# Optimization experiments

Measured on AMD Instinct MI355X. Metric: run time of the kernel, lower is better.

The kernel has to match this reference:

```python
import jax, jax.numpy as jnp
import numpy as np

DIM, DEPTH, DH, H, NLAT, MAXT, MAXF, FFM = 1024, 6, 64, 8, 64, 8, 16, 4
INNER = DH * H

def _ln(x, w, b, eps=1e-5):
    m = jnp.mean(x, axis=-1, keepdims=True)
    v = jnp.mean(jnp.square(x - m), axis=-1, keepdims=True)
    return (x - m) * jax.lax.rsqrt(v + eps) * w + b

def setup_inputs() -> dict:
    key = jax.random.key(0)
    ks = iter(jax.random.split(key, 32))
    s = 0.02
    d = {
        'x': jax.random.normal(next(ks), (2, 8, 16, 256, DIM), jnp.float32),
        'latents': jax.random.normal(next(ks), (NLAT, DIM), jnp.float32),
        'frame_emb': jax.random.normal(next(ks), (MAXF, DIM), jnp.float32),
        'media_emb': jax.random.normal(next(ks), (MAXT, 1, DIM), jnp.float32),
        'lnm_w': jnp.ones((DEPTH, DIM)), 'lnm_b': jnp.zeros((DEPTH, DIM)),
        'lnl_w': jnp.ones((DEPTH, DIM)), 'lnl_b': jnp.zeros((DEPTH, DIM)),
        'Wq': jax.random.normal(next(ks), (DEPTH, DIM, INNER), jnp.float32) * s,
        'Wkv': jax.random.normal(next(ks), (DEPTH, DIM, 2 * INNER), jnp.float32) * s,
        'Wo': jax.random.normal(next(ks), (DEPTH, INNER, DIM), jnp.float32) * s,
        'ffln_w': jnp.ones((DEPTH, DIM)), 'ffln_b': jnp.zeros((DEPTH, DIM)),
        'W1': jax.random.normal(next(ks), (DEPTH, DIM, FFM * DIM), jnp.float32) * s,
        'b1': jnp.zeros((DEPTH, FFM * DIM)),
        'W2': jax.random.normal(next(ks), (DEPTH, FFM * DIM, DIM), jnp.float32) * s,
        'b2': jnp.zeros((DEPTH, DIM)),
        'fln_w': jnp.ones((DIM,)), 'fln_b': jnp.zeros((DIM,)),
    }
    return d

def _split_heads(t):  # b T n (h d) -> b h T n d
    b, T, n, _ = t.shape
    return t.reshape(b, T, n, H, DH).transpose(0, 3, 1, 2, 4)

def _forward(x, latents, frame_emb, media_emb, lnm_w, lnm_b, lnl_w, lnl_b,
             Wq, Wkv, Wo, ffln_w, ffln_b, W1, b1, W2, b2, fln_w, fln_b):
    b, T, F, v, d = x.shape
    x = x + frame_emb[:F][None, None, :, None, :]      # b T F v d
    x = x.reshape(b, T, F * v, d)
    x = x + media_emb[:T]                              # [T,1,d] broadcasts
    lat = jnp.broadcast_to(latents, (b, T, NLAT, d))
    scale = DH ** -0.5
    for i in range(DEPTH):
        xn = _ln(x, lnm_w[i], lnm_b[i])
        ln_lat = _ln(lat, lnl_w[i], lnl_b[i])
        q = _split_heads(ln_lat @ Wq[i]) * scale       # b h T n2 dh
        kv = jnp.concatenate([xn, ln_lat], axis=2) @ Wkv[i]
        k, vv = jnp.split(kv, 2, axis=-1)
        k, vv = _split_heads(k), _split_heads(vv)      # b h T (n1+n2) dh
        sim = jnp.einsum('bhtid,bhtjd->bhtij', q, k)
        sim = sim - jax.lax.stop_gradient(jnp.max(sim, axis=-1, keepdims=True))
        attn = jax.nn.softmax(sim, axis=-1)
        o = jnp.einsum('bhtij,bhtjd->bhtid', attn, vv)
        o = o.transpose(0, 2, 3, 1, 4).reshape(b, T, NLAT, INNER)
        lat = (o @ Wo[i]) + lat
        h = _ln(lat, ffln_w[i], ffln_b[i])
        h = jax.nn.gelu(h @ W1[i] + b1[i], approximate=False) @ W2[i] + b2[i]
        lat = h + lat
    return _ln(lat, fln_w, fln_b)

def reference(x, latents, frame_emb, media_emb, lnm_w, lnm_b, lnl_w, lnl_b,
              Wq, Wkv, Wo, ffln_w, ffln_b, W1, b1, W2, b2, fln_w, fln_b):
    return _forward(x, latents, frame_emb, media_emb, lnm_w, lnm_b, lnl_w, lnl_b,
                    Wq, Wkv, Wo, ffln_w, ffln_b, W1, b1, W2, b2, fln_w, fln_b)
```

## Files before the change

kernel.cpp:

```cpp
#include <hip/hip_runtime.h>
#include <math.h>


#define DIM   1024
#define DEPTH 6
#define HEADS 8
#define NLAT  64
#define INNER 512
#define FFD   4096
#define XROWS 65536
#define LROWS 1024
#define NBT   16
#define QKVN  1536

typedef __attribute__((ext_vector_type(8))) short bf16x8;
typedef __attribute__((ext_vector_type(4))) float f32x4;

#define WAITV(n) asm volatile("s_waitcnt vmcnt(" #n ")" ::: "memory")

__device__ __forceinline__ short f2bf(float f) {
  union { float f; unsigned u; } v; v.f = f;
  unsigned r = v.u + 0x7fffu + ((v.u >> 16) & 1u);
  return (short)(r >> 16);
}

__device__ __forceinline__ void gload16(const void* g, void* l) {
  __builtin_amdgcn_global_load_lds(
      (const __attribute__((address_space(1))) unsigned int*)g,
      (__attribute__((address_space(3))) unsigned int*)l, 16, 0, 0);
}

__device__ __forceinline__ f32x4 zero_f4() { f32x4 z; z[0]=0.f; z[1]=0.f; z[2]=0.f; z[3]=0.f; return z; }
__device__ __forceinline__ bf16x8 zero_b8() { bf16x8 z;
#pragma unroll
  for (int e=0;e<8;e++) z[e]=0; return z; }

__global__ __launch_bounds__(256)
void prep_kernel(const float* __restrict__ x, const float* __restrict__ fe,
                 const float* __restrict__ me, short* __restrict__ xhat)
{
  int lane = threadIdx.x & 63;
  int r = blockIdx.x*4 + (threadIdx.x >> 6);
  int f = (r >> 8) & 15, tt = (r >> 12) & 7;
  const float4* xp = (const float4*)(x + (size_t)r*DIM);
  const float4* fp = (const float4*)(fe + (size_t)f*DIM);
  const float4* mp = (const float4*)(me + (size_t)tt*DIM);
  float y[16];
  float s = 0.f, sq = 0.f;
#pragma unroll
  for (int k = 0; k < 4; k++) {
    float4 xv = xp[k*64 + lane], fv = fp[k*64 + lane], mv = mp[k*64 + lane];
    float a0 = xv.x+fv.x+mv.x, a1 = xv.y+fv.y+mv.y, a2 = xv.z+fv.z+mv.z, a3 = xv.w+fv.w+mv.w;
    y[k*4+0]=a0; y[k*4+1]=a1; y[k*4+2]=a2; y[k*4+3]=a3;
    s += a0+a1+a2+a3; sq += a0*a0+a1*a1+a2*a2+a3*a3;
  }
#pragma unroll
  for (int off = 32; off >= 1; off >>= 1) {
    s  += __shfl_xor(s,  off, 64);
    sq += __shfl_xor(sq, off, 64);
  }
  float mean = s * (1.0f/DIM);
  float var  = sq * (1.0f/DIM) - mean*mean;
  float rs = rsqrtf(var + 1e-5f);
  short4* op = (short4*)(xhat + (size_t)r*DIM);
#pragma unroll
  for (int k = 0; k < 4; k++) {
    short4 o;
    o.x = f2bf((y[k*4+0]-mean)*rs); o.y = f2bf((y[k*4+1]-mean)*rs);
    o.z = f2bf((y[k*4+2]-mean)*rs); o.w = f2bf((y[k*4+3]-mean)*rs);
    op[k*64 + lane] = o;
  }
}

__device__ __forceinline__ void reduce2(float& s, float& sq, float* sh) {
#pragma unroll
  for (int off = 32; off >= 1; off >>= 1) {
    s  += __shfl_xor(s,  off, 64);
    sq += __shfl_xor(sq, off, 64);
  }
  int t = threadIdx.x;
  if ((t & 63) == 0) { sh[(t >> 6)*2] = s; sh[(t >> 6)*2 + 1] = sq; }
  __syncthreads();
  s  = sh[0] + sh[2] + sh[4] + sh[6];
  sq = sh[1] + sh[3] + sh[5] + sh[7];
}

template<bool OBF>
__global__ __launch_bounds__(256)
void ln_kernel(const float* __restrict__ in, const float* __restrict__ w,
               const float* __restrict__ b, void* __restrict__ outp)
{
  __shared__ float sh[8];
  int r = blockIdx.x, t = threadIdx.x;
  float4 xv = ((const float4*)(in + (size_t)r*DIM))[t];
  float s = xv.x+xv.y+xv.z+xv.w;
  float sq = xv.x*xv.x+xv.y*xv.y+xv.z*xv.z+xv.w*xv.w;
  reduce2(s, sq, sh);
  float mean = s*(1.0f/DIM), var = sq*(1.0f/DIM) - mean*mean;
  float rs = rsqrtf(var + 1e-5f);
  float4 wv = ((const float4*)w)[t], bv = ((const float4*)b)[t];
  float o0 = (xv.x-mean)*rs*wv.x + bv.x;
  float o1 = (xv.y-mean)*rs*wv.y + bv.y;
  float o2 = (xv.z-mean)*rs*wv.z + bv.z;
  float o3 = (xv.w-mean)*rs*wv.w + bv.w;
  if (OBF) {
    short4 o; o.x=f2bf(o0); o.y=f2bf(o1); o.z=f2bf(o2); o.w=f2bf(o3);
    ((short4*)((short*)outp + (size_t)r*DIM))[t] = o;
  } else {
    float4 o; o.x=o0; o.y=o1; o.z=o2; o.w=o3;
    ((float4*)((float*)outp + (size_t)r*DIM))[t] = o;
  }
}

__global__ __launch_bounds__(256)
void latinit_kernel(const float* __restrict__ latents, float* __restrict__ lat)
{
  int idx = blockIdx.x * 256 + threadIdx.x;
  int e = idx << 2;
  int row = e >> 10;
  int i = row & 63;
  int col = e & 1023;
  *(float4*)(lat + e) = *(const float4*)(latents + (i << 10) + col);
}

__global__ __launch_bounds__(256)
void kvbp_kernel(const float* __restrict__ lnm_b, const float* __restrict__ Wkv,
                 float* __restrict__ kvb_part)
{
  int z = blockIdx.x, i = blockIdx.y, t = threadIdx.x;
  const float* W = Wkv + (size_t)i*DIM*DIM;
  const float* bv = lnm_b + (size_t)i*DIM;
  float acc0=0,acc1=0,acc2=0,acc3=0;
  for (int k = z*64; k < z*64+64; k++) {
    float b = bv[k];
    const float* Wr = W + (size_t)k*DIM;
    acc0 += b * Wr[t];       acc1 += b * Wr[t+256];
    acc2 += b * Wr[t+512];   acc3 += b * Wr[t+768];
  }
  float* o = kvb_part + (size_t)(i*16 + z)*DIM;
  o[t] = acc0; o[t+256] = acc1; o[t+512] = acc2; o[t+768] = acc3;
}

__global__ __launch_bounds__(256)
void kvbred_kernel(const float* __restrict__ kvb_part, float* __restrict__ kvb)
{
  int i = blockIdx.x, t = threadIdx.x;
#pragma unroll
  for (int j = 0; j < 4; j++) {
    int col = t + j*256;
    float s = 0.f;
#pragma unroll
    for (int z = 0; z < 16; z++) s += kvb_part[(size_t)(i*16 + z)*DIM + col];
    kvb[i*DIM + col] = s;
  }
}

__global__ __launch_bounds__(256)
void tcast_all_kernel(const float* __restrict__ Wkv, const float* __restrict__ Wq,
                      const float* __restrict__ Wo, const float* __restrict__ W1,
                      const float* __restrict__ W2, const float* __restrict__ lnmw,
                      short* __restrict__ Wkv_f, short* __restrict__ qkvW,
                      short* __restrict__ Wo_h, short* __restrict__ W1_h,
                      short* __restrict__ W2_h)
{
  int b = blockIdx.x;
  const float* src; short* dst; const float* fold = nullptr; float scale = 1.0f;
  int K, N, bx, ntx;
  if (b < 256)      { src=Wkv; dst=Wkv_f; fold=lnmw; K=1024; N=1024; bx=b;      ntx=16; }
  else if (b < 384) { src=Wq;  dst=qkvW;  scale=0.125f; K=1024; N=512; bx=b-256; ntx=8; }
  else if (b < 640) { src=Wkv; dst=qkvW+512*1024; K=1024; N=1024; bx=b-384; ntx=16; }
  else if (b < 768) { src=Wo;  dst=Wo_h;  K=512;  N=1024; bx=b-640; ntx=16; }
  else if (b < 1792){ src=W1;  dst=W1_h;  K=1024; N=4096; bx=b-768; ntx=64; }
  else              { src=W2;  dst=W2_h;  K=4096; N=1024; bx=b-1792; ntx=16; }
  int n0 = (bx % ntx)*64, k0 = (bx / ntx)*64;
  __shared__ float tile[64][65];
  int t = threadIdx.x;
#pragma unroll
  for (int i = 0; i < 16; i++) {
    int rr = (t >> 6) + i*4, cc = t & 63;
    float v = src[(size_t)(k0+rr)*N + n0 + cc] * scale;
    if (fold) v *= fold[k0 + rr];
    tile[rr][cc] = v;
  }
  __syncthreads();
#pragma unroll
  for (int i = 0; i < 16; i++) {
    int nn = (t >> 6) + i*4, kk = t & 63;
    dst[(size_t)(n0+nn)*K + k0 + kk] = f2bf(tile[kk][nn]);
  }
}

__global__ __launch_bounds__(512, 1)
void gemm256p_kernel(const short* __restrict__ A, const short* __restrict__ Bt,
                     short* __restrict__ C, const float* __restrict__ bias,
                     int M, int N, int K)
{
  __shared__ __align__(16) short lds[65536];
  char* ldsc = (char*)lds;
  const int t = threadIdx.x, lane = t & 63, wid = t >> 6;
  const int wm = wid >> 2, wn = wid & 3;

  const int nwg = gridDim.x * gridDim.y;
  const int id = blockIdx.y * gridDim.x + blockIdx.x;
  const int work = (id & 7) * (nwg >> 3) + (id >> 3);
  const int bn = work % gridDim.x, bm = work / gridDim.x;
  const int m0 = bm * 256, n0 = bn * 256;

  f32x4 acc[8][4];
#pragma unroll
  for (int m=0;m<8;m++)
#pragma unroll
    for (int n=0;n<4;n++) acc[m][n] = zero_f4();

  auto stage = [&](int tile, int mat, int half) {
    const short* src = mat ? Bt : A;
    const int base0 = (mat ? n0 : m0) + half*128;
    char* dbase = ldsc + (mat*32768 + (tile & 1)*16384 + half*8192)*2;
#pragma unroll
    for (int i = 0; i < 2; i++) {
      int chunk = i*512 + t;
      int row_h = chunk >> 3, slot = chunk & 7;
      int ss = slot ^ (row_h & 7);
      gload16(src + (size_t)(base0 + row_h)*K + tile*64 + ss*8,
              dbase + (i*512 + (wid << 6))*16);
    }
  };
  auto LDA = [&](int buf, int mf, int ks) -> bf16x8 {
    int row = wm*128 + mf*16 + (lane & 15);
    int slot = (ks*4 + (lane >> 4)) ^ (row & 7);
    return *(const bf16x8*)(ldsc + (buf*16384 + row*64)*2 + slot*16);
  };
  auto LDB = [&](int buf, int nf, int ks) -> bf16x8 {
    int row = wn*64 + nf*16 + (lane & 15);
    int slot = (ks*4 + (lane >> 4)) ^ (row & 7);
    return *(const bf16x8*)(ldsc + (32768 + buf*16384 + row*64)*2 + slot*16);
  };

#define PHASE(BUF, Q, STAGE_STMT, GATE) do {                               \
    if ((Q) == 0) {                                                        \
      _Pragma("unroll") for (int n_=0;n_<4;n_++)                           \
        _Pragma("unroll") for (int k_=0;k_<2;k_++)                         \
          bfr[n_][k_] = LDB((BUF), n_, k_);                                \
    }                                                                      \
    _Pragma("unroll") for (int i_=0;i_<2;i_++)                             \
      _Pragma("unroll") for (int k_=0;k_<2;k_++)                           \
        afr[i_][k_] = LDA((BUF), 2*(Q)+i_, k_);                            \
    STAGE_STMT;                                                            \
    GATE;                                                                  \
    __builtin_amdgcn_sched_barrier(0);                                     \
    __builtin_amdgcn_s_barrier();                                          \
    asm volatile("s_waitcnt lgkmcnt(0)" ::: "memory");                     \
    __builtin_amdgcn_sched_barrier(0);                                     \
    __builtin_amdgcn_s_setprio(1);                                         \
    _Pragma("unroll") for (int k_=0;k_<2;k_++)                             \
      _Pragma("unroll") for (int i_=0;i_<2;i_++)                           \
        _Pragma("unroll") for (int n_=0;n_<4;n_++)                         \
          acc[2*(Q)+i_][n_] = __builtin_amdgcn_mfma_f32_16x16x32_bf16(     \
              afr[i_][k_], bfr[n_][k_], acc[2*(Q)+i_][n_], 0, 0, 0);       \
    __builtin_amdgcn_s_setprio(0);                                         \
    __builtin_amdgcn_sched_barrier(0);                                     \
    __builtin_amdgcn_s_barrier();                                          \
  } while (0)

  const int NU = K >> 7;
  stage(0, 0, 0); stage(0, 0, 1); stage(0, 1, 0); stage(0, 1, 1);
  stage(1, 1, 0); stage(1, 1, 1);
  WAITV(4);
  __builtin_amdgcn_sched_barrier(0);
  __builtin_amdgcn_s_barrier();

#pragma unroll 1
  for (int u = 0; u < NU; ++u) {
    const int t0 = 2*u, t1 = t0 + 1;
    const bool more = (u + 1 < NU);
    bf16x8 bfr[4][2], afr[2][2];
    PHASE(0, 0, stage(t1, 0, 0),               (void)0);
    PHASE(0, 1, stage(t1, 0, 1),               (void)0);
    PHASE(0, 2, if (more) stage(t0+2, 1, 0),   (void)0);
    PHASE(0, 3, if (more) stage(t0+2, 1, 1),   WAITV(4));
    PHASE(1, 0, if (more) stage(t0+2, 0, 0),   (void)0);
    PHASE(1, 1, if (more) stage(t0+2, 0, 1),   (void)0);
    PHASE(1, 2, if (more) stage(t1+2, 1, 0),   (void)0);
    PHASE(1, 3, if (more) stage(t1+2, 1, 1),   WAITV(4));
  }
#undef PHASE

  const int g = lane >> 4;
#pragma unroll
  for (int m=0;m<8;m++) {
#pragma unroll
    for (int n=0;n<4;n++) {
#pragma unroll
      for (int r=0;r<4;r++) {
        int mm = m0 + wm*128 + m*16 + g*4 + r;
        int nn = n0 + wn*64 + n*16 + (lane & 15);
        float v = acc[m][n][r] + bias[nn];
        C[(size_t)mm*N + nn] = f2bf(v);
      }
    }
  }
}

template<int EPI, bool HAS_BIAS>
__global__ __launch_bounds__(256, 2)
void gemm_kernel(const short* __restrict__ A, const short* __restrict__ Bt,
                 void* __restrict__ Cout, const float* __restrict__ bias,
                 int M, int N, int K, int ldk)
{
  __shared__ __align__(16) short As[128*64];
  __shared__ __align__(16) short Bs[128*64];
  const int t = threadIdx.x;
  const int lane = t & 63, w = t >> 6;
  const int m0 = blockIdx.x * 128, n0 = blockIdx.y * 128;
  const int wr = (w >> 1) * 64, wc = (w & 1) * 64;
  const short* Ap = A + (size_t)blockIdx.z * K;
  const short* Btp = Bt + (size_t)blockIdx.z * K;

  f32x4 acc[4][4];
#pragma unroll
  for (int i=0;i<4;i++)
#pragma unroll
    for (int j=0;j<4;j++) acc[i][j] = zero_f4();

  for (int kt = 0; kt < K; kt += 64) {
#pragma unroll
    for (int i = 0; i < 4; i++) {
      int chunk = i*256 + t;
      int row = chunk >> 3, slot = chunk & 7;
      int ss = slot ^ (row & 7);
      gload16(Ap + (size_t)(m0 + row)*ldk + kt + ss*8,
              (char*)As + (i*256 + (w<<6))*16);
    }
#pragma unroll
    for (int i = 0; i < 4; i++) {
      int chunk = i*256 + t;
      int row = chunk >> 3, slot = chunk & 7;
      int ss = slot ^ (row & 7);
      gload16(Btp + (size_t)(n0 + row)*ldk + kt + ss*8,
              (char*)Bs + (i*256 + (w<<6))*16);
    }
    __syncthreads();

#pragma unroll
    for (int ks = 0; ks < 2; ks++) {
      bf16x8 af[4], bfr[4];
#pragma unroll
      for (int i=0;i<4;i++) {
        int row = wr + i*16 + (lane & 15);
        int slot = (ks*4 + (lane >> 4)) ^ (row & 7);
        af[i] = *(const bf16x8*)((const char*)As + row*128 + slot*16);
        int nrow = wc + i*16 + (lane & 15);
        int nslot = (ks*4 + (lane >> 4)) ^ (nrow & 7);
        bfr[i] = *(const bf16x8*)((const char*)Bs + nrow*128 + nslot*16);
      }
#pragma unroll
      for (int i=0;i<4;i++)
#pragma unroll
        for (int j=0;j<4;j++)
          acc[i][j] = __builtin_amdgcn_mfma_f32_16x16x32_bf16(af[i], bfr[j], acc[i][j], 0, 0, 0);
    }
    __syncthreads();
  }

  const int g = lane >> 4;
#pragma unroll
  for (int i=0;i<4;i++) {
#pragma unroll
    for (int j=0;j<4;j++) {
#pragma unroll
      for (int r=0;r<4;r++) {
        int m = m0 + wr + i*16 + g*4 + r;
        int n = n0 + wc + j*16 + (lane & 15);
        float v = acc[i][j][r];
        if (EPI == 0) {
          if (HAS_BIAS) v += bias[n];
          ((short*)Cout)[(size_t)m*N + n] = f2bf(v);
        } else if (EPI == 1) {
          if (HAS_BIAS) v += bias[n];
          float gl = 0.5f * v * (1.0f + erff(v * 0.70710678f));
          ((short*)Cout)[(size_t)m*N + n] = f2bf(gl);
        } else if (EPI == 2) {
          if (HAS_BIAS) v += bias[n];
          float* o = (float*)Cout + (size_t)m*N + n;
          *o += v;
        } else {
          ((float*)Cout)[(size_t)blockIdx.z*M*N + (size_t)m*N + n] = v;
        }
      }
    }
  }
}

__global__ __launch_bounds__(256)
void w2red_kernel(const float* __restrict__ part, const float* __restrict__ b2,
                  float* __restrict__ lat)
{
  int idx = blockIdx.x * 256 + threadIdx.x;
  float4 a = ((float4*)lat)[idx];
  float4 bb = ((const float4*)b2)[idx & 255];
  a.x += bb.x; a.y += bb.y; a.z += bb.z; a.w += bb.w;
#pragma unroll
  for (int z = 0; z < 4; z++) {
    float4 p = ((const float4*)(part + (size_t)z*LROWS*DIM))[idx];
    a.x += p.x; a.y += p.y; a.z += p.z; a.w += p.w;
  }
  ((float4*)lat)[idx] = a;
}

__global__ __launch_bounds__(256, 2)
void attn_part_kernel(const short* __restrict__ qkvlat, const short* __restrict__ kvbuf,
                      float* __restrict__ part_O, float* __restrict__ part_m,
                      float* __restrict__ part_l)
{
  __shared__ __align__(16) short q_sh[64*64];
  __shared__ __align__(16) short K_sh[128*64];
  __shared__ __align__(16) short VT_sh[64*128];
  __shared__ __align__(16) short P_sh[64*132];

  const int t = threadIdx.x, lane = t & 63, w = t >> 6;
  const int bid = blockIdx.x;
  const int s = bid & 7, bh = bid >> 3;
  const int h = bh & 7, bt = bh >> 3;

  {
    const short* qsrc = qkvlat + (size_t)(bt*64)*QKVN + h*64;
#pragma unroll
    for (int i = 0; i < 2; i++) {
      int chunk = i*256 + t;
      int row = chunk >> 3, slot = chunk & 7;
      gload16(qsrc + (size_t)row*QKVN + ((slot ^ (row & 7))*8),
              (char*)q_sh + (i*256 + (w<<6))*16);
    }
  }

  float m_run[4], l_run[4];
#pragma unroll
  for (int r=0;r<4;r++){ m_run[r] = -1e30f; l_run[r] = 0.f; }
  f32x4 oacc[4];
#pragma unroll
  for (int j=0;j<4;j++) oacc[j] = zero_f4();

  const int nch = (s == 7) ? 5 : 4;
  for (int c5 = 0; c5 < nch; c5++) {
    __syncthreads();
    const bool isLat = (c5 == 4);
    const int jv = isLat ? 4 : 8;
    const short* kbase; int kstride, valid;
    if (!isLat) {
      kbase = kvbuf + ((size_t)bt*4096 + (s*4 + c5)*128)*DIM + h*64;
      kstride = DIM; valid = 128;
    } else {
      kbase = qkvlat + (size_t)(bt*64)*QKVN + 512 + h*64;
      kstride = QKVN; valid = 64;
    }
    const short* vbase = kbase + 512;

#pragma unroll
    for (int i = 0; i < 4; i++) {
      int chunk = i*256 + t;
      int row = chunk >> 3, slot = chunk & 7;
      gload16(kbase + (size_t)row*kstride + ((slot ^ (row & 7))*8),
              (char*)K_sh + (i*256 + (w<<6))*16);
    }
#pragma unroll
    for (int i = 0; i < 4; i++) {
      int c = i*256 + t;
      int row = c >> 3, slot = c & 7;
      bf16x8 v = (row < valid) ? *(const bf16x8*)(vbase + (size_t)row*kstride + slot*8) : zero_b8();
      int kslot = row >> 3;
#pragma unroll
      for (int e=0;e<8;e++) {
        int dh = slot*8 + e;
        VT_sh[dh*128 + ((kslot ^ (dh & 7))*8) + (row & 7)] = v[e];
      }
    }
    __syncthreads();

    f32x4 sacc[8];
#pragma unroll
    for (int j=0;j<8;j++) sacc[j] = zero_f4();
#pragma unroll
    for (int ks=0; ks<2; ks++) {
      int arow = w*16 + (lane & 15);
      int aslot = (ks*4 + (lane >> 4)) ^ (arow & 7);
      bf16x8 af = *(const bf16x8*)((const char*)q_sh + arow*128 + aslot*16);
#pragma unroll
      for (int j=0;j<8;j++) {
        int brow = j*16 + (lane & 15);
        int bslot = (ks*4 + (lane >> 4)) ^ (brow & 7);
        bf16x8 bv = *(const bf16x8*)((const char*)K_sh + brow*128 + bslot*16);
        sacc[j] = __builtin_amdgcn_mfma_f32_16x16x32_bf16(af, bv, sacc[j], 0, 0, 0);
      }
    }

    float mx[4];
#pragma unroll
    for (int r=0;r<4;r++) mx[r] = -1e30f;
#pragma unroll
    for (int j=0;j<8;j++) {
      if (j < jv) {
#pragma unroll
        for (int r=0;r<4;r++) mx[r] = fmaxf(mx[r], sacc[j][r]);
      }
    }
#pragma unroll
    for (int m2=1; m2<16; m2<<=1) {
#pragma unroll
      for (int r=0;r<4;r++) mx[r] = fmaxf(mx[r], __shfl_xor(mx[r], m2, 64));
    }
    float alpha[4], rowsum[4];
#pragma unroll
    for (int r=0;r<4;r++) {
      float nm = fmaxf(m_run[r], mx[r]);
      alpha[r] = __expf(m_run[r] - nm);
      m_run[r] = nm;
      rowsum[r] = 0.f;
    }
#pragma unroll
    for (int j=0;j<8;j++) {
#pragma unroll
      for (int r=0;r<4;r++) {
        float p = 0.f;
        if (j < jv) { p = __expf(sacc[j][r] - m_run[r]); rowsum[r] += p; }
        P_sh[(w*16 + (lane>>4)*4 + r)*132 + j*16 + (lane & 15)] = f2bf(p);
      }
    }
#pragma unroll
    for (int m2=1; m2<16; m2<<=1) {
#pragma unroll
      for (int r=0;r<4;r++) rowsum[r] += __shfl_xor(rowsum[r], m2, 64);
    }
#pragma unroll
    for (int r=0;r<4;r++) l_run[r] = l_run[r]*alpha[r] + rowsum[r];
#pragma unroll
    for (int j=0;j<4;j++) {
#pragma unroll
      for (int r=0;r<4;r++) oacc[j][r] *= alpha[r];
    }
    __syncthreads();

#pragma unroll
    for (int ks=0; ks<4; ks++) {
      int prow = w*16 + (lane & 15);
      bf16x8 af = *(const bf16x8*)((const char*)P_sh + prow*264 + ks*64 + (lane >> 4)*16);
#pragma unroll
      for (int j=0;j<4;j++) {
        int dh = j*16 + (lane & 15);
        int kslot = (ks*4 + (lane >> 4)) ^ (dh & 7);
        bf16x8 bv = *(const bf16x8*)((const char*)VT_sh + dh*256 + kslot*16);
        oacc[j] = __builtin_amdgcn_mfma_f32_16x16x32_bf16(af, bv, oacc[j], 0, 0, 0);
      }
    }
  }

  {
    float* Ob = part_O + (size_t)bid*4096;
    int rbase = w*16 + (lane>>4)*4;
#pragma unroll
    for (int j=0;j<4;j++) {
#pragma unroll
      for (int r=0;r<4;r++)
        Ob[(rbase + r)*64 + j*16 + (lane & 15)] = oacc[j][r];
    }
    if ((lane & 15) == 0) {
#pragma unroll
      for (int r=0;r<4;r++) {
        part_m[(size_t)bid*64 + rbase + r] = m_run[r];
        part_l[(size_t)bid*64 + rbase + r] = l_run[r];
      }
    }
  }
}

__global__ __launch_bounds__(256)
void attn_combine_kernel(const float* __restrict__ part_O, const float* __restrict__ part_m,
                         const float* __restrict__ part_l, short* __restrict__ obuf)
{
  int bh = blockIdx.x, t = threadIdx.x;
  int q = t >> 2, c0 = (t & 3) * 16;
  int bt = bh >> 3, h = bh & 7;
  float m8[8], w8[8];
  float mmax = -1e30f;
#pragma unroll
  for (int s=0;s<8;s++) { m8[s] = part_m[(size_t)(bh*8+s)*64 + q]; mmax = fmaxf(mmax, m8[s]); }
  float lt = 0.f;
#pragma unroll
  for (int s=0;s<8;s++) { w8[s] = __expf(m8[s] - mmax); lt += w8[s] * part_l[(size_t)(bh*8+s)*64 + q]; }
  float inv = 1.0f / lt;
  float4 acc[4];
#pragma unroll
  for (int u=0;u<4;u++) { acc[u].x=0.f; acc[u].y=0.f; acc[u].z=0.f; acc[u].w=0.f; }
#pragma unroll
  for (int s=0;s<8;s++) {
    const float4* Ob = (const float4*)(part_O + ((size_t)(bh*8+s)*64 + q)*64 + c0);
#pragma unroll
    for (int u=0;u<4;u++) {
      float4 v = Ob[u];
      acc[u].x += w8[s]*v.x; acc[u].y += w8[s]*v.y;
      acc[u].z += w8[s]*v.z; acc[u].w += w8[s]*v.w;
    }
  }
  short* ob = obuf + (size_t)(bt*64 + q)*INNER + h*64 + c0;
#pragma unroll
  for (int u=0;u<4;u++) {
    short4 o;
    o.x = f2bf(acc[u].x*inv); o.y = f2bf(acc[u].y*inv);
    o.z = f2bf(acc[u].z*inv); o.w = f2bf(acc[u].w*inv);
    ((short4*)ob)[u] = o;
  }
}

extern "C" void kernel_launch(void* const* d_in, const int* in_sizes, int n_in,
                              void* d_out, int out_size, void* d_ws, size_t ws_size,
                              hipStream_t stream)
{
  (void)in_sizes; (void)n_in; (void)out_size; (void)ws_size;
  const float* x        = (const float*)d_in[0];
  const float* latents  = (const float*)d_in[1];
  const float* frame_e  = (const float*)d_in[2];
  const float* media_e  = (const float*)d_in[3];
  const float* lnm_w    = (const float*)d_in[4];
  const float* lnm_b    = (const float*)d_in[5];
  const float* lnl_w    = (const float*)d_in[6];
  const float* lnl_b    = (const float*)d_in[7];
  const float* Wq       = (const float*)d_in[8];
  const float* Wkv      = (const float*)d_in[9];
  const float* Wo       = (const float*)d_in[10];
  const float* ffln_w   = (const float*)d_in[11];
  const float* ffln_b   = (const float*)d_in[12];
  const float* W1       = (const float*)d_in[13];
  const float* b1       = (const float*)d_in[14];
  const float* W2       = (const float*)d_in[15];
  const float* b2       = (const float*)d_in[16];
  const float* fln_w    = (const float*)d_in[17];
  const float* fln_b    = (const float*)d_in[18];
  float* out = (float*)d_out;

  char* ws = (char*)d_ws;
  size_t off = 0;
  short* xhat   = (short*)(ws + off); off += (size_t)XROWS*DIM*2;
  short* kvbuf  = (short*)(ws + off); off += (size_t)XROWS*DIM*2;
  short* Wkv_f  = (short*)(ws + off); off += (size_t)DIM*DIM*2;
  short* qkvW   = (short*)(ws + off); off += (size_t)QKVN*DIM*2;
  short* Wo_h   = (short*)(ws + off); off += (size_t)INNER*DIM*2;
  short* W1_h   = (short*)(ws + off); off += (size_t)DIM*FFD*2;
  short* W2_h   = (short*)(ws + off); off += (size_t)FFD*DIM*2;
  float* kvb    = (float*)(ws + off); off += (size_t)DEPTH*DIM*4;
  float* kvbp   = (float*)(ws + off); off += (size_t)DEPTH*16*DIM*4;
  float* lat    = (float*)(ws + off); off += (size_t)LROWS*DIM*4;
  short* lnlat  = (short*)(ws + off); off += (size_t)LROWS*DIM*2;
  short* qkvlat = (short*)(ws + off); off += (size_t)LROWS*QKVN*2;
  short* obuf   = (short*)(ws + off); off += (size_t)LROWS*INNER*2;
  short* hbuf   = (short*)(ws + off); off += (size_t)LROWS*DIM*2;
  short* h1     = (short*)(ws + off); off += (size_t)LROWS*FFD*2;
  float* w2part = (float*)(ws + off); off += (size_t)4*LROWS*DIM*4;
  float* part_O = (float*)(ws + off); off += (size_t)1024*64*64*4;
  float* part_m = (float*)(ws + off); off += (size_t)1024*64*4;
  float* part_l = (float*)(ws + off); off += (size_t)1024*64*4;

  prep_kernel<<<XROWS/4, 256, 0, stream>>>(x, frame_e, media_e, xhat);
  latinit_kernel<<<1024, 256, 0, stream>>>(latents, lat);
  kvbp_kernel<<<dim3(16, DEPTH), 256, 0, stream>>>(lnm_b, Wkv, kvbp);
  kvbred_kernel<<<DEPTH, 256, 0, stream>>>(kvbp, kvb);

  for (int i = 0; i < DEPTH; i++) {
    tcast_all_kernel<<<2816, 256, 0, stream>>>(
        Wkv + (size_t)i*DIM*DIM, Wq + (size_t)i*DIM*INNER, Wo + (size_t)i*INNER*DIM,
        W1 + (size_t)i*DIM*FFD, W2 + (size_t)i*FFD*DIM, lnm_w + (size_t)i*DIM,
        Wkv_f, qkvW, Wo_h, W1_h, W2_h);

    ln_kernel<true><<<LROWS, 256, 0, stream>>>(lat, lnl_w + i*DIM, lnl_b + i*DIM, lnlat);
    gemm_kernel<0,false><<<dim3(LROWS/128, QKVN/128), 256, 0, stream>>>(
        lnlat, qkvW, qkvlat, nullptr, LROWS, QKVN, DIM, DIM);
    gemm256p_kernel<<<dim3(DIM/256, XROWS/256), 512, 0, stream>>>(
        xhat, Wkv_f, kvbuf, kvb + i*DIM, XROWS, DIM, DIM);
    attn_part_kernel<<<1024, 256, 0, stream>>>(qkvlat, kvbuf, part_O, part_m, part_l);
    attn_combine_kernel<<<128, 256, 0, stream>>>(part_O, part_m, part_l, obuf);
    gemm_kernel<2,false><<<dim3(LROWS/128, DIM/128), 256, 0, stream>>>(
        obuf, Wo_h, lat, nullptr, LROWS, DIM, INNER, INNER);
    ln_kernel<true><<<LROWS, 256, 0, stream>>>(lat, ffln_w + i*DIM, ffln_b + i*DIM, hbuf);
    gemm_kernel<1,true><<<dim3(LROWS/128, FFD/128), 256, 0, stream>>>(
        hbuf, W1_h, h1, b1 + (size_t)i*FFD, LROWS, FFD, DIM, DIM);
    gemm_kernel<4,false><<<dim3(LROWS/128, DIM/128, 4), 256, 0, stream>>>(
        h1, W2_h, w2part, nullptr, LROWS, DIM, DIM, FFD);
    w2red_kernel<<<1024, 256, 0, stream>>>(w2part, b2 + (size_t)i*DIM, lat);
  }
  ln_kernel<false><<<LROWS, 256, 0, stream>>>(lat, fln_w, fln_b, out);
}
```

Baseline: 2.082 ms.

## Fuse KV GEMM, QKV GEMM and next-layer weight cast into one mega kernel

```diff
diff --git a/kernel.cpp b/kernel.cpp
--- a/kernel.cpp
+++ b/kernel.cpp
@@ -113,14 +113,27 @@
 }
 
 __global__ __launch_bounds__(256)
-void latinit_kernel(const float* __restrict__ latents, float* __restrict__ lat)
-{
-  int idx = blockIdx.x * 256 + threadIdx.x;
-  int e = idx << 2;
-  int row = e >> 10;
-  int i = row & 63;
-  int col = e & 1023;
-  *(float4*)(lat + e) = *(const float4*)(latents + (i << 10) + col);
+void latinit_ln_kernel(const float* __restrict__ latents, const float* __restrict__ w,
+                       const float* __restrict__ b, float* __restrict__ lat,
+                       short* __restrict__ lnlat)
+{
+  __shared__ float sh[8];
+  int r = blockIdx.x, t = threadIdx.x;
+  int i = r & 63;
+  float4 a = ((const float4*)(latents + (size_t)i*DIM))[t];
+  ((float4*)(lat + (size_t)r*DIM))[t] = a;
+  float s = a.x+a.y+a.z+a.w;
+  float sq = a.x*a.x+a.y*a.y+a.z*a.z+a.w*a.w;
+  reduce2(s, sq, sh);
+  float mean = s*(1.0f/DIM), var = sq*(1.0f/DIM) - mean*mean;
+  float rs = rsqrtf(var + 1e-5f);
+  float4 wv = ((const float4*)w)[t], bv = ((const float4*)b)[t];
+  short4 o;
+  o.x = f2bf((a.x-mean)*rs*wv.x + bv.x);
+  o.y = f2bf((a.y-mean)*rs*wv.y + bv.y);
+  o.z = f2bf((a.z-mean)*rs*wv.z + bv.z);
+  o.w = f2bf((a.w-mean)*rs*wv.w + bv.w);
+  ((short4*)(lnlat + (size_t)r*DIM))[t] = o;
 }
 
 __global__ __launch_bounds__(256)
@@ -155,6 +168,25 @@
   }
 }
 
+struct TcastArgs {
+  const float* src; short* dst; const float* fold; float scale; int K, N, bx, ntx;
+};
+
+__device__ __forceinline__ TcastArgs tcast_map(
+    int b, const float* Wkv, const float* Wq, const float* Wo, const float* W1,
+    const float* W2, const float* lnmw, short* Wkv_f, short* qkvW,
+    short* Wo_h, short* W1_h, short* W2_h)
+{
+  TcastArgs a; a.fold = nullptr; a.scale = 1.0f;
+  if (b < 256)      { a.src=Wkv; a.dst=Wkv_f; a.fold=lnmw; a.K=1024; a.N=1024; a.bx=b;      a.ntx=16; }
+  else if (b < 384) { a.src=Wq;  a.dst=qkvW;  a.scale=0.125f; a.K=1024; a.N=512; a.bx=b-256; a.ntx=8; }
+  else if (b < 640) { a.src=Wkv; a.dst=qkvW+512*1024; a.K=1024; a.N=1024; a.bx=b-384; a.ntx=16; }
+  else if (b < 768) { a.src=Wo;  a.dst=Wo_h;  a.K=512;  a.N=1024; a.bx=b-640; a.ntx=16; }
+  else if (b < 1792){ a.src=W1;  a.dst=W1_h;  a.K=1024; a.N=4096; a.bx=b-768; a.ntx=64; }
+  else              { a.src=W2;  a.dst=W2_h;  a.K=4096; a.N=1024; a.bx=b-1792; a.ntx=16; }
+  return a;
+}
+
 __global__ __launch_bounds__(256)
 void tcast_all_kernel(const float* __restrict__ Wkv, const float* __restrict__ Wq,
                       const float* __restrict__ Wo, const float* __restrict__ W1,
@@ -163,47 +195,36 @@
                       short* __restrict__ Wo_h, short* __restrict__ W1_h,
                       short* __restrict__ W2_h)
 {
-  int b = blockIdx.x;
-  const float* src; short* dst; const float* fold = nullptr; float scale = 1.0f;
-  int K, N, bx, ntx;
-  if (b < 256)      { src=Wkv; dst=Wkv_f; fold=lnmw; K=1024; N=1024; bx=b;      ntx=16; }
-  else if (b < 384) { src=Wq;  dst=qkvW;  scale=0.125f; K=1024; N=512; bx=b-256; ntx=8; }
-  else if (b < 640) { src=Wkv; dst=qkvW+512*1024; K=1024; N=1024; bx=b-384; ntx=16; }
-  else if (b < 768) { src=Wo;  dst=Wo_h;  K=512;  N=1024; bx=b-640; ntx=16; }
-  else if (b < 1792){ src=W1;  dst=W1_h;  K=1024; N=4096; bx=b-768; ntx=64; }
-  else              { src=W2;  dst=W2_h;  K=4096; N=1024; bx=b-1792; ntx=16; }
-  int n0 = (bx % ntx)*64, k0 = (bx / ntx)*64;
+  TcastArgs a = tcast_map(blockIdx.x, Wkv, Wq, Wo, W1, W2, lnmw, Wkv_f, qkvW, Wo_h, W1_h, W2_h);
+  int n0 = (a.bx % a.ntx)*64, k0 = (a.bx / a.ntx)*64;
   __shared__ float tile[64][65];
   int t = threadIdx.x;
 #pragma unroll
   for (int i = 0; i < 16; i++) {
     int rr = (t >> 6) + i*4, cc = t & 63;
-    float v = src[(size_t)(k0+rr)*N + n0 + cc] * scale;
-    if (fold) v *= fold[k0 + rr];
+    float v = a.src[(size_t)(k0+rr)*a.N + n0 + cc] * a.scale;
+    if (a.fold) v *= a.fold[k0 + rr];
     tile[rr][cc] = v;
   }
   __syncthreads();
 #pragma unroll
   for (int i = 0; i < 16; i++) {
     int nn = (t >> 6) + i*4, kk = t & 63;
-    dst[(size_t)(n0+nn)*K + k0 + kk] = f2bf(tile[kk][nn]);
-  }
-}
-
-__global__ __launch_bounds__(512, 1)
-void gemm256p_kernel(const short* __restrict__ A, const short* __restrict__ Bt,
-                     short* __restrict__ C, const float* __restrict__ bias,
-                     int M, int N, int K)
-{
-  __shared__ __align__(16) short lds[65536];
-  char* ldsc = (char*)lds;
+    a.dst[(size_t)(n0+nn)*a.K + k0 + kk] = f2bf(tile[kk][nn]);
+  }
+}
+
+
+__device__ __forceinline__ void kv256_path(
+    const short* __restrict__ A, const short* __restrict__ Bt,
+    short* __restrict__ C, const float* __restrict__ bias, int b, char* ldsc)
+{
   const int t = threadIdx.x, lane = t & 63, wid = t >> 6;
   const int wm = wid >> 2, wn = wid & 3;
-
-  const int nwg = gridDim.x * gridDim.y;
-  const int id = blockIdx.y * gridDim.x + blockIdx.x;
-  const int work = (id & 7) * (nwg >> 3) + (id >> 3);
-  const int bn = work % gridDim.x, bm = work / gridDim.x;
+  const int K = DIM, N = DIM;
+
+  const int work = (b & 7) * 128 + (b >> 3);
+  const int bn = work & 3, bm = work >> 2;
   const int m0 = bm * 256, n0 = bn * 256;
 
   f32x4 acc[8][4];
@@ -277,11 +298,11 @@
     PHASE(0, 0, stage(t1, 0, 0),               (void)0);
     PHASE(0, 1, stage(t1, 0, 1),               (void)0);
     PHASE(0, 2, if (more) stage(t0+2, 1, 0),   (void)0);
-    PHASE(0, 3, if (more) stage(t0+2, 1, 1),   WAITV(4));
+    PHASE(0, 3, if (more) stage(t0+2, 1, 1),   if (more) { WAITV(4); } else { WAITV(0); });
     PHASE(1, 0, if (more) stage(t0+2, 0, 0),   (void)0);
     PHASE(1, 1, if (more) stage(t0+2, 0, 1),   (void)0);
     PHASE(1, 2, if (more) stage(t1+2, 1, 0),   (void)0);
-    PHASE(1, 3, if (more) stage(t1+2, 1, 1),   WAITV(4));
+    PHASE(1, 3, if (more) stage(t1+2, 1, 1),   if (more) { WAITV(4); });
   }
 #undef PHASE
 
@@ -298,6 +319,118 @@
         C[(size_t)mm*N + nn] = f2bf(v);
       }
     }
+  }
+}
+
+__device__ __forceinline__ void qkv_path(
+    const short* __restrict__ A, const short* __restrict__ Bt,
+    short* __restrict__ C, int q, char* ldsc)
+{
+  const int t = threadIdx.x, lane = t & 63, wid = t >> 6;
+  const int m0 = (q & 7) * 128, n0 = (q >> 3) * 128;
+  const int wr = (wid >> 2) * 64, wc = (wid & 3) * 32;
+  char* As = ldsc;
+  char* Bs = ldsc + 16384;
+
+  f32x4 acc[4][2];
+#pragma unroll
+  for (int i=0;i<4;i++)
+#pragma unroll
+    for (int j=0;j<2;j++) acc[i][j] = zero_f4();
+
+  for (int kt = 0; kt < DIM; kt += 64) {
+#pragma unroll
+    for (int i = 0; i < 2; i++) {
+      int chunk = i*512 + t;
+      int row = chunk >> 3, slot = chunk & 7;
+      int ss = slot ^ (row & 7);
+      gload16(A + (size_t)(m0 + row)*DIM + kt + ss*8, As + (i*512 + (wid<<6))*16);
+    }
+#pragma unroll
+    for (int i = 0; i < 2; i++) {
+      int chunk = i*512 + t;
+      int row = chunk >> 3, slot = chunk & 7;
+      int ss = slot ^ (row & 7);
+      gload16(Bt + (size_t)(n0 + row)*DIM + kt + ss*8, Bs + (i*512 + (wid<<6))*16);
+    }
+    __syncthreads();
+#pragma unroll
+    for (int ks = 0; ks < 2; ks++) {
+      bf16x8 af[4], bfr[2];
+#pragma unroll
+      for (int i=0;i<4;i++) {
+        int row = wr + i*16 + (lane & 15);
+        int slot = (ks*4 + (lane >> 4)) ^ (row & 7);
+        af[i] = *(const bf16x8*)(As + row*128 + slot*16);
+      }
+#pragma unroll
+      for (int j=0;j<2;j++) {
+        int row = wc + j*16 + (lane & 15);
+        int slot = (ks*4 + (lane >> 4)) ^ (row & 7);
+        bfr[j] = *(const bf16x8*)(Bs + row*128 + slot*16);
+      }
+#pragma unroll
+      for (int i=0;i<4;i++)
+#pragma unroll
+        for (int j=0;j<2;j++)
+          acc[i][j] = __builtin_amdgcn_mfma_f32_16x16x32_bf16(af[i], bfr[j], acc[i][j], 0, 0, 0);
+    }
+    __syncthreads();
+  }
+
+  const int g = lane >> 4;
+#pragma unroll
+  for (int i=0;i<4;i++) {
+#pragma unroll
+    for (int j=0;j<2;j++) {
+#pragma unroll
+      for (int r=0;r<4;r++) {
+        int mm = m0 + wr + i*16 + g*4 + r;
+        int nn = n0 + wc + j*16 + (lane & 15);
+        C[(size_t)mm*QKVN + nn] = f2bf(acc[i][j][r]);
+      }
+    }
+  }
+}
+
+__device__ __forceinline__ void tcast_path(const TcastArgs& a, float* tile65)
+{
+  int n0 = (a.bx % a.ntx)*64, k0 = (a.bx / a.ntx)*64;
+  int t = threadIdx.x;
+#pragma unroll
+  for (int i = 0; i < 8; i++) {
+    int rr = (t >> 6) + i*8, cc = t & 63;
+    float v = a.src[(size_t)(k0+rr)*a.N + n0 + cc] * a.scale;
+    if (a.fold) v *= a.fold[k0 + rr];
+    tile65[rr*65 + cc] = v;
+  }
+  __syncthreads();
+#pragma unroll
+  for (int i = 0; i < 8; i++) {
+    int nn = (t >> 6) + i*8, kk = t & 63;
+    a.dst[(size_t)(n0+nn)*a.K + k0 + kk] = f2bf(tile65[kk*65 + nn]);
+  }
+}
+
+__global__ __launch_bounds__(512, 2)
+void mega_kernel(const short* __restrict__ xhat, const short* __restrict__ Wkvf,
+                 const float* __restrict__ kvb_i, short* __restrict__ kvbuf,
+                 const short* __restrict__ lnlat, const short* __restrict__ qkvW,
+                 short* __restrict__ qkvlat,
+                 const float* nWkv, const float* nWq, const float* nWo,
+                 const float* nW1, const float* nW2, const float* nlnmw,
+                 short* dWkvf, short* dqkvW, short* dWo, short* dW1, short* dW2)
+{
+  __shared__ __align__(16) short lds[65536];
+  int b = blockIdx.x;
+  if (b < 1024) {
+    kv256_path(xhat, Wkvf, kvbuf, kvb_i, b, (char*)lds);
+  } else if (b < 1120) {
+    qkv_path(lnlat, qkvW, qkvlat, b - 1024, (char*)lds);
+  } else {
+    TcastArgs a = tcast_map(b - 1120, nWkv, nWq, nWo, nW1, nW2, nlnmw,
+                            dWkvf, dqkvW, dWo, dW1, dW2);
+    tcast_path(a, (float*)lds);
   }
 }
 
@@ -372,10 +505,7 @@
         int m = m0 + wr + i*16 + g*4 + r;
         int n = n0 + wc + j*16 + (lane & 15);
         float v = acc[i][j][r];
-        if (EPI == 0) {
-          if (HAS_BIAS) v += bias[n];
-          ((short*)Cout)[(size_t)m*N + n] = f2bf(v);
-        } else if (EPI == 1) {
+        if (EPI == 1) {
           if (HAS_BIAS) v += bias[n];
           float gl = 0.5f * v * (1.0f + erff(v * 0.70710678f));
           ((short*)Cout)[(size_t)m*N + n] = f2bf(gl);
@@ -391,20 +521,41 @@
   }
 }
 
+template<bool LAST>
 __global__ __launch_bounds__(256)
-void w2red_kernel(const float* __restrict__ part, const float* __restrict__ b2,
-                  float* __restrict__ lat)
-{
-  int idx = blockIdx.x * 256 + threadIdx.x;
+void w2red_ln_kernel(const float* __restrict__ part, const float* __restrict__ b2,
+                     float* __restrict__ lat, const float* __restrict__ w,
+                     const float* __restrict__ bb, void* __restrict__ dst)
+{
+  __shared__ float sh[8];
+  int r = blockIdx.x, t = threadIdx.x;
+  int idx = r*256 + t;
   float4 a = ((float4*)lat)[idx];
-  float4 bb = ((const float4*)b2)[idx & 255];
-  a.x += bb.x; a.y += bb.y; a.z += bb.z; a.w += bb.w;
+  float4 b4 = ((const float4*)b2)[t];
+  a.x += b4.x; a.y += b4.y; a.z += b4.z; a.w += b4.w;
 #pragma unroll
   for (int z = 0; z < 4; z++) {
     float4 p = ((const float4*)(part + (size_t)z*LROWS*DIM))[idx];
     a.x += p.x; a.y += p.y; a.z += p.z; a.w += p.w;
   }
   ((float4*)lat)[idx] = a;
+  float s = a.x+a.y+a.z+a.w;
+  float sq = a.x*a.x+a.y*a.y+a.z*a.z+a.w*a.w;
+  reduce2(s, sq, sh);
+  float mean = s*(1.0f/DIM), var = sq*(1.0f/DIM) - mean*mean;
+  float rs = rsqrtf(var + 1e-5f);
+  float4 wv = ((const float4*)w)[t], bv = ((const float4*)bb)[t];
+  float o0 = (a.x-mean)*rs*wv.x + bv.x;
+  float o1 = (a.y-mean)*rs*wv.y + bv.y;
+  float o2 = (a.z-mean)*rs*wv.z + bv.z;
+  float o3 = (a.w-mean)*rs*wv.w + bv.w;
+  if (LAST) {
+    float4 o; o.x=o0; o.y=o1; o.z=o2; o.w=o3;
+    ((float4*)((float*)dst + (size_t)r*DIM))[t] = o;
+  } else {
+    short4 o; o.x=f2bf(o0); o.y=f2bf(o1); o.z=f2bf(o2); o.w=f2bf(o3);
+    ((short4*)((short*)dst + (size_t)r*DIM))[t] = o;
+  }
 }
 
 __global__ __launch_bounds__(256, 2)
@@ -640,11 +791,14 @@
   size_t off = 0;
   short* xhat   = (short*)(ws + off); off += (size_t)XROWS*DIM*2;
   short* kvbuf  = (short*)(ws + off); off += (size_t)XROWS*DIM*2;
-  short* Wkv_f  = (short*)(ws + off); off += (size_t)DIM*DIM*2;
-  short* qkvW   = (short*)(ws + off); off += (size_t)QKVN*DIM*2;
-  short* Wo_h   = (short*)(ws + off); off += (size_t)INNER*DIM*2;
-  short* W1_h   = (short*)(ws + off); off += (size_t)DIM*FFD*2;
-  short* W2_h   = (short*)(ws + off); off += (size_t)FFD*DIM*2;
+  short* Wkvf_b[2]; short* qkvW_b[2]; short* Wo_b[2]; short* W1_b[2]; short* W2_b[2];
+  for (int j = 0; j < 2; j++) {
+    Wkvf_b[j] = (short*)(ws + off); off += (size_t)DIM*DIM*2;
+    qkvW_b[j] = (short*)(ws + off); off += (size_t)QKVN*DIM*2;
+    Wo_b[j]   = (short*)(ws + off); off += (size_t)INNER*DIM*2;
+    W1_b[j]   = (short*)(ws + off); off += (size_t)DIM*FFD*2;
+    W2_b[j]   = (short*)(ws + off); off += (size_t)FFD*DIM*2;
+  }
   float* kvb    = (float*)(ws + off); off += (size_t)DEPTH*DIM*4;
   float* kvbp   = (float*)(ws + off); off += (size_t)DEPTH*16*DIM*4;
   float* lat    = (float*)(ws + off); off += (size_t)LROWS*DIM*4;
@@ -659,31 +813,35 @@
   float* part_l = (float*)(ws + off); off += (size_t)1024*64*4;
 
   prep_kernel<<<XROWS/4, 256, 0, stream>>>(x, frame_e, media_e, xhat);
-  latinit_kernel<<<1024, 256, 0, stream>>>(latents, lat);
+  latinit_ln_kernel<<<LROWS, 256, 0, stream>>>(latents, lnl_w, lnl_b, lat, lnlat);
   kvbp_kernel<<<dim3(16, DEPTH), 256, 0, stream>>>(lnm_b, Wkv, kvbp);
   kvbred_kernel<<<DEPTH, 256, 0, stream>>>(kvbp, kvb);
+  tcast_all_kernel<<<2816, 256, 0, stream>>>(
+      Wkv, Wq, Wo, W1, W2, lnm_w, Wkvf_b[0], qkvW_b[0], Wo_b[0], W1_b[0], W2_b[0]);
 
   for (int i = 0; i < DEPTH; i++) {
-    tcast_all_kernel<<<2816, 256, 0, stream>>>(
-        Wkv + (size_t)i*DIM*DIM, Wq + (size_t)i*DIM*INNER, Wo + (size_t)i*INNER*DIM,
-        W1 + (size_t)i*DIM*FFD, W2 + (size_t)i*FFD*DIM, lnm_w + (size_t)i*DIM,
-        Wkv_f, qkvW, Wo_h, W1_h, W2_h);
-
-    ln_kernel<true><<<LROWS, 256, 0, stream>>>(lat, lnl_w + i*DIM, lnl_b + i*DIM, lnlat);
-    gemm_kernel<0,false><<<dim3(LROWS/128, QKVN/128), 256, 0, stream>>>(
-        lnlat, qkvW, qkvlat, nullptr, LROWS, QKVN, DIM, DIM);
-    gemm256p_kernel<<<dim3(DIM/256, XROWS/256), 512, 0, stream>>>(
-        xhat, Wkv_f, kvbuf, kvb + i*DIM, XROWS, DIM, DIM);
+    const int cur = i & 1, nxt = (i + 1) & 1;
+    const int ni = (i + 1 < DEPTH) ? (i + 1) : 0;
+    mega_kernel<<<(i < DEPTH-1) ? 3936 : 1120, 512, 0, stream>>>(
+        xhat, Wkvf_b[cur], kvb + i*DIM, kvbuf, lnlat, qkvW_b[cur], qkvlat,
+        Wkv + (size_t)ni*DIM*DIM, Wq + (size_t)ni*DIM*INNER, Wo + (size_t)ni*INNER*DIM,
+        W1 + (size_t)ni*DIM*FFD, W2 + (size_t)ni*FFD*DIM, lnm_w + (size_t)ni*DIM,
+        Wkvf_b[nxt], qkvW_b[nxt], Wo_b[nxt], W1_b[nxt], W2_b[nxt]);
+
     attn_part_kernel<<<1024, 256, 0, stream>>>(qkvlat, kvbuf, part_O, part_m, part_l);
     attn_combine_kernel<<<128, 256, 0, stream>>>(part_O, part_m, part_l, obuf);
     gemm_kernel<2,false><<<dim3(LROWS/128, DIM/128), 256, 0, stream>>>(
-        obuf, Wo_h, lat, nullptr, LROWS, DIM, INNER, INNER);
+        obuf, Wo_b[cur], lat, nullptr, LROWS, DIM, INNER, INNER);
     ln_kernel<true><<<LROWS, 256, 0, stream>>>(lat, ffln_w + i*DIM, ffln_b + i*DIM, hbuf);
     gemm_kernel<1,true><<<dim3(LROWS/128, FFD/128), 256, 0, stream>>>(
-        hbuf, W1_h, h1, b1 + (size_t)i*FFD, LROWS, FFD, DIM, DIM);
+        hbuf, W1_b[cur], h1, b1 + (size_t)i*FFD, LROWS, FFD, DIM, DIM);
     gemm_kernel<4,false><<<dim3(LROWS/128, DIM/128, 4), 256, 0, stream>>>(
-        h1, W2_h, w2part, nullptr, LROWS, DIM, DIM, FFD);
-    w2red_kernel<<<1024, 256, 0, stream>>>(w2part, b2 + (size_t)i*DIM, lat);
-  }
-  ln_kernel<false><<<LROWS, 256, 0, stream>>>(lat, fln_w, fln_b, out);
-}
+        h1, W2_b[cur], w2part, nullptr, LROWS, DIM, DIM, FFD);
+    if (i < DEPTH-1)
+      w2red_ln_kernel<false><<<LROWS, 256, 0, stream>>>(
+          w2part, b2 + (size_t)i*DIM, lat, lnl_w + (i+1)*DIM, lnl_b + (i+1)*DIM, lnlat);
+    else
+      w2red_ln_kernel<true><<<LROWS, 256, 0, stream>>>(
+          w2part, b2 + (size_t)i*DIM, lat, fln_w, fln_b, out);
+  }
+}
```

After: 2.170 ms. 4.2% more time.
